# Optimization experiments

Measured on AMD Instinct MI355X. Metric: run time of the kernel, lower is better.

Reference implementation:

```python
import jax, jax.numpy as jnp
import numpy as np

FRAME_LENGTH = 50
MAX_PEOPLE = 3
NEG_INF = -1e10


def _build_smooth_mask():
    tp = FRAME_LENGTH * MAX_PEOPLE
    m = np.zeros((tp, tp), dtype=np.int32)
    for t in range(1, FRAME_LENGTH - 1):
        lo, hi = (t - 1) * MAX_PEOPLE, (t + 1) * MAX_PEOPLE
        m[lo:hi, lo:hi] = 1
    return jnp.asarray(m)


def setup_inputs() -> dict:
    key = jax.random.key(0)
    k1, k2, k3 = jax.random.split(key, 3)
    BS, T, P, H = 32, 50, 3, 4
    TP = T * P
    return {
        "idx": jax.random.randint(k1, (BS, TP), 0, 2),
        "idx_mask": jnp.ones((BS, TP), dtype=jnp.float32),
        "idx_kp": jax.random.randint(jax.random.fold_in(k1, 1), (BS, T, P), 0, 2),
        "points_2d": jax.random.normal(k2, (BS, TP, 44, 2), dtype=jnp.float32),
        "attn": jax.random.normal(k3, (BS, H, TP, TP), dtype=jnp.float32),
    }


def reference(idx, idx_mask, idx_kp, points_2d, attn):
    BS, T, P = idx_kp.shape
    TP = T * P
    kp = points_2d.reshape(BS, TP, 44, 2)
    # pairwise L1 distance summed over keypoints and coords: (BS, TP, TP)
    loss_kp = jnp.sum(jnp.abs(kp[:, None, :, :, :] - kp[:, :, None, :, :]), axis=(3, 4))
    smooth_mask = _build_smooth_mask()  # (TP, TP)
    attn_masked = jnp.where(smooth_mask[None, None] == 0, jnp.asarray(NEG_INF, attn.dtype), attn)
    atten3 = jax.nn.softmax(attn_masked, axis=-1)  # (BS, H, TP, TP)
    smooth_loss = loss_kp[:, None, :, :] * atten3  # (BS, H, TP, TP)
    idx_f = idx.astype(smooth_loss.dtype)
    pair = idx_f[:, None, :, None] * idx_f[:, None, None, :]  # (BS, 1, TP, TP)
    H = attn.shape[1]
    num = jnp.sum(smooth_loss * pair)  # broadcasting over H == masked sum over repeated idx_
    den = 1.0 + H * jnp.sum(pair)      # idx_ was repeated H times before summation
    return num / den
```

## Files before the change

kernel.cpp:

```cpp
#include <hip/hip_runtime.h>
#include <math.h>

#define BS    32
#define T_    50
#define P_    3
#define TP    150
#define HEADS 4
#define NKP   88

__global__ __launch_bounds__(64) void smooth_rows(
    const int*   __restrict__ idx,
    const float* __restrict__ kp,
    const float* __restrict__ attn,
    float*       __restrict__ partials)
{
    int bi = blockIdx.x;
    int b  = bi / TP;
    int i  = bi - b * TP;
    int lane = threadIdx.x;

    if (idx[b * TP + i] == 0) {
        if (lane == 0) partials[bi] = 0.f;
        return;
    }

    const float* kpb = kp + (size_t)b * TP * NKP;

    __shared__ __align__(16) float s_kpi[NKP];
    __shared__ float s_lw[9];

    if (lane < NKP / 2)
        ((float2*)s_kpi)[lane] = ((const float2*)(kpb + i * NKP))[lane];
    __syncthreads();

    if (i < (T_ - 1) * P_) {
        int f   = i / P_;
        int flo = f > 0 ? f - 1 : 0;
        int fhi = f < T_ - 2 ? f + 1 : T_ - 2;
        int jlo = flo * P_;
        int nj  = (fhi - flo + 1) * P_;

        float a0 = s_kpi[lane];
        float a1 = (lane < NKP - 64) ? s_kpi[lane + 64] : 0.f;

        float d[9];
        #pragma unroll
        for (int jj = 0; jj < 9; ++jj) {
            int j = jlo + (jj < nj ? jj : 0);
            const float* kpj = kpb + j * NKP;
            float t = fabsf(kpj[lane] - a0);
            if (lane < NKP - 64) t += fabsf(kpj[lane + 64] - a1);
            d[jj] = t;
        }
        #pragma unroll
        for (int jj = 0; jj < 9; ++jj) {
            #pragma unroll
            for (int off = 32; off; off >>= 1) d[jj] += __shfl_down(d[jj], off);
        }
        if (lane == 0) {
            #pragma unroll
            for (int jj = 0; jj < 9; ++jj) s_lw[jj] = d[jj];
        }
        __syncthreads();

        int h  = lane >> 4;
        int jx = lane & 15;
        bool act = jx < nj;
        int  j  = jlo + (act ? jx : 0);
        float idxj = act ? (float)idx[b * TP + j] : 0.f;
        float a = act ? attn[(((size_t)b * HEADS + h) * TP + i) * TP + j]
                      : -INFINITY;
        float m = a;
        #pragma unroll
        for (int off = 8; off; off >>= 1) m = fmaxf(m, __shfl_xor(m, off));
        float e = act ? expf(a - m) : 0.f;
        float w = act ? e * s_lw[jx] * idxj : 0.f;
        #pragma unroll
        for (int off = 8; off; off >>= 1) { e += __shfl_xor(e, off); w += __shfl_xor(w, off); }
        float ch = w / e;
        float c0 = __shfl(ch, 0);
        float c1 = __shfl(ch, 16);
        float c2 = __shfl(ch, 32);
        float c3 = __shfl(ch, 48);
        if (lane == 0) partials[bi] = c0 + c1 + c2 + c3;
    } else {
        float acc = 0.f;
        for (int j = lane; j < TP; j += 64) {
            if (idx[b * TP + j]) {
                const float4* kpj4 = (const float4*)(kpb + j * NKP);
                const float4* kpi4 = (const float4*)s_kpi;
                float s = 0.f;
                #pragma unroll
                for (int c = 0; c < NKP / 4; ++c) {
                    float4 q = kpj4[c];
                    float4 p = kpi4[c];
                    s += fabsf(q.x - p.x) + fabsf(q.y - p.y)
                       + fabsf(q.z - p.z) + fabsf(q.w - p.w);
                }
                acc += s;
            }
        }
        #pragma unroll
        for (int off = 32; off; off >>= 1) acc += __shfl_down(acc, off);
        if (lane == 0) partials[bi] = acc * ((float)HEADS / (float)TP);
    }
}

__global__ __launch_bounds__(256) void smooth_reduce(
    const int*   __restrict__ idx,
    const float* __restrict__ partials,
    float*       __restrict__ out)
{
    int tid = threadIdx.x;

    float s = 0.f;
    for (int k = tid; k < BS * TP; k += 256) s += partials[k];
    #pragma unroll
    for (int off = 32; off; off >>= 1) s += __shfl_down(s, off);
    __shared__ float s_red[4];
    if ((tid & 63) == 0) s_red[tid >> 6] = s;

    __shared__ int s_sb[BS];
    int b = tid >> 3;
    int l = tid & 7;
    int si = 0;
    for (int k = l; k < TP; k += 8) si += idx[b * TP + k];
    #pragma unroll
    for (int off = 4; off; off >>= 1) si += __shfl_down(si, off, 8);
    if (l == 0) s_sb[b] = si;
    __syncthreads();

    if (tid == 0) {
        float num = s_red[0] + s_red[1] + s_red[2] + s_red[3];
        float tot = 0.f;
        for (int bb = 0; bb < BS; ++bb) {
            float v = (float)s_sb[bb];
            tot += v * v;
        }
        out[0] = num / (1.0f + (float)HEADS * tot);
    }
}

extern "C" void kernel_launch(void* const* d_in, const int* in_sizes, int n_in,
                              void* d_out, int out_size, void* d_ws, size_t ws_size,
                              hipStream_t stream)
{
    const int*   idx  = (const int*)  d_in[0];
    const float* kp   = (const float*)d_in[3];
    const float* attn = (const float*)d_in[4];
    float* out      = (float*)d_out;
    float* partials = (float*)d_ws;

    smooth_rows<<<BS * TP, 64, 0, stream>>>(idx, kp, attn, partials);
    smooth_reduce<<<1, 256, 0, stream>>>(idx, partials, out);
}
```

Measured before the change: 83.73 us.

## Process one frame (three rows) per block, reusing neighbor keypoints in registers

Each block now handles a whole frame of three person rows instead of one row, so the nine neighbor keypoint vectors are loaded once into registers and reused across the three rows. The shared-memory staging and its barrier are replaced by xor-shuffle reductions and register selection. The per-batch idx sum-of-squares now comes from the last-frame block, which simplifies the reduce kernel. The grid shrinks threefold, which lowers parallelism and launch count but raises per-block work and register pressure.

```diff
diff --git a/kernel.cpp b/kernel.cpp
--- a/kernel.cpp
+++ b/kernel.cpp
@@ -7,136 +7,165 @@
 #define TP    150
 #define HEADS 4
 #define NKP   88
+#define NFRM  50
 
-__global__ __launch_bounds__(64) void smooth_rows(
+__global__ __launch_bounds__(64) void smooth_frames(
     const int*   __restrict__ idx,
     const float* __restrict__ kp,
     const float* __restrict__ attn,
     float*       __restrict__ partials)
 {
-    int bi = blockIdx.x;
-    int b  = bi / TP;
-    int i  = bi - b * TP;
+    int bf   = blockIdx.x;
+    int b    = bf / NFRM;
+    int f    = bf - b * NFRM;
     int lane = threadIdx.x;
 
-    if (idx[b * TP + i] == 0) {
-        if (lane == 0) partials[bi] = 0.f;
+    const int*   idxb = idx + b * TP;
+    const float* kpb  = kp + (size_t)b * TP * NKP;
+
+    __shared__ __align__(16) float s_kp[3 * NKP];
+
+    if (f == NFRM - 1) {
+        int si = 0;
+        for (int k = lane; k < TP; k += 64) si += idxb[k];
+        #pragma unroll
+        for (int off = 32; off; off >>= 1) si += __shfl_down(si, off);
+
+        for (int c = lane; c < 3 * NKP / 4; c += 64)
+            ((float4*)s_kp)[c] = ((const float4*)(kpb + (TP - 3) * NKP))[c];
+        __syncthreads();
+
+        int id0 = idxb[TP - 3], id1 = idxb[TP - 2], id2 = idxb[TP - 1];
+
+        float acc0 = 0.f, acc1 = 0.f, acc2 = 0.f;
+        for (int j = lane; j < TP; j += 64) {
+            if (idxb[j]) {
+                const float4* kj = (const float4*)(kpb + j * NKP);
+                const float4* p0 = (const float4*)(s_kp);
+                const float4* p1 = (const float4*)(s_kp + NKP);
+                const float4* p2 = (const float4*)(s_kp + 2 * NKP);
+                float s0 = 0.f, s1 = 0.f, s2 = 0.f;
+                #pragma unroll
+                for (int c = 0; c < NKP / 4; ++c) {
+                    float4 q = kj[c];
+                    float4 a = p0[c];
+                    float4 d = p1[c];
+                    float4 e = p2[c];
+                    s0 += fabsf(q.x - a.x) + fabsf(q.y - a.y) + fabsf(q.z - a.z) + fabsf(q.w - a.w);
+                    s1 += fabsf(q.x - d.x) + fabsf(q.y - d.y) + fabsf(q.z - d.z) + fabsf(q.w - d.w);
+                    s2 += fabsf(q.x - e.x) + fabsf(q.y - e.y) + fabsf(q.z - e.z) + fabsf(q.w - e.w);
+                }
+                acc0 += s0; acc1 += s1; acc2 += s2;
+            }
+        }
+        float acc = (id0 ? acc0 : 0.f) + (id1 ? acc1 : 0.f) + (id2 ? acc2 : 0.f);
+        #pragma unroll
+        for (int off = 32; off; off >>= 1) acc += __shfl_down(acc, off);
+
+        if (lane == 0) {
+            partials[bf] = acc * ((float)HEADS / (float)TP);
+            float fs = (float)si;
+            partials[BS * NFRM + b] = fs * fs;
+        }
         return;
     }
 
-    const float* kpb = kp + (size_t)b * TP * NKP;
+    int i0  = P_ * f;
+    int id0 = idxb[i0], id1 = idxb[i0 + 1], id2 = idxb[i0 + 2];
+    if (!(id0 | id1 | id2)) {
+        if (lane == 0) partials[bf] = 0.f;
+        return;
+    }
 
-    __shared__ __align__(16) float s_kpi[NKP];
-    __shared__ float s_lw[9];
+    int flo = f > 0 ? f - 1 : 0;
+    int fhi = f < T_ - 2 ? f + 1 : T_ - 2;
+    int jlo = flo * P_;
+    int nj  = (fhi - flo + 1) * P_;
 
-    if (lane < NKP / 2)
-        ((float2*)s_kpi)[lane] = ((const float2*)(kpb + i * NKP))[lane];
-    __syncthreads();
+    bool hi = lane < NKP - 64;
+    float kj0[9], kj1[9];
+    #pragma unroll
+    for (int jj = 0; jj < 9; ++jj) {
+        int j = jlo + (jj < nj ? jj : 0);
+        kj0[jj] = kpb[j * NKP + lane];
+        kj1[jj] = hi ? kpb[j * NKP + 64 + lane] : 0.f;
+    }
 
-    if (i < (T_ - 1) * P_) {
-        int f   = i / P_;
-        int flo = f > 0 ? f - 1 : 0;
-        int fhi = f < T_ - 2 ? f + 1 : T_ - 2;
-        int jlo = flo * P_;
-        int nj  = (fhi - flo + 1) * P_;
+    int  h    = lane >> 4;
+    int  jx   = lane & 15;
+    bool act  = jx < nj;
+    float idxj = act ? (float)idxb[jlo + jx] : 0.f;
 
-        float a0 = s_kpi[lane];
-        float a1 = (lane < NKP - 64) ? s_kpi[lane + 64] : 0.f;
+    float acc = 0.f;
+    #pragma unroll
+    for (int ii = 0; ii < 3; ++ii) {
+        int idi = (ii == 0) ? id0 : (ii == 1) ? id1 : id2;
+        if (!idi) continue;
+        int i = i0 + ii;
+
+        float a0 = kpb[i * NKP + lane];
+        float a1 = hi ? kpb[i * NKP + 64 + lane] : 0.f;
 
         float d[9];
         #pragma unroll
-        for (int jj = 0; jj < 9; ++jj) {
-            int j = jlo + (jj < nj ? jj : 0);
-            const float* kpj = kpb + j * NKP;
-            float t = fabsf(kpj[lane] - a0);
-            if (lane < NKP - 64) t += fabsf(kpj[lane + 64] - a1);
-            d[jj] = t;
-        }
+        for (int jj = 0; jj < 9; ++jj)
+            d[jj] = fabsf(kj0[jj] - a0) + fabsf(kj1[jj] - a1);
         #pragma unroll
         for (int jj = 0; jj < 9; ++jj) {
             #pragma unroll
-            for (int off = 32; off; off >>= 1) d[jj] += __shfl_down(d[jj], off);
+            for (int off = 32; off; off >>= 1) d[jj] += __shfl_xor(d[jj], off);
         }
-        if (lane == 0) {
-            #pragma unroll
-            for (int jj = 0; jj < 9; ++jj) s_lw[jj] = d[jj];
-        }
-        __syncthreads();
+        float lw = d[0];
+        lw = (jx == 1) ? d[1] : lw;
+        lw = (jx == 2) ? d[2] : lw;
+        lw = (jx == 3) ? d[3] : lw;
+        lw = (jx == 4) ? d[4] : lw;
+        lw = (jx == 5) ? d[5] : lw;
+        lw = (jx == 6) ? d[6] : lw;
+        lw = (jx == 7) ? d[7] : lw;
+        lw = (jx == 8) ? d[8] : lw;
 
-        int h  = lane >> 4;
-        int jx = lane & 15;
-        bool act = jx < nj;
-        int  j  = jlo + (act ? jx : 0);
-        float idxj = act ? (float)idx[b * TP + j] : 0.f;
-        float a = act ? attn[(((size_t)b * HEADS + h) * TP + i) * TP + j]
+        float a = act ? attn[(((size_t)(b * HEADS + h)) * TP + i) * TP + (jlo + jx)]
                       : -INFINITY;
         float m = a;
         #pragma unroll
         for (int off = 8; off; off >>= 1) m = fmaxf(m, __shfl_xor(m, off));
         float e = act ? expf(a - m) : 0.f;
-        float w = act ? e * s_lw[jx] * idxj : 0.f;
+        float w = e * lw * idxj;
         #pragma unroll
         for (int off = 8; off; off >>= 1) { e += __shfl_xor(e, off); w += __shfl_xor(w, off); }
-        float ch = w / e;
-        float c0 = __shfl(ch, 0);
-        float c1 = __shfl(ch, 16);
-        float c2 = __shfl(ch, 32);
-        float c3 = __shfl(ch, 48);
-        if (lane == 0) partials[bi] = c0 + c1 + c2 + c3;
-    } else {
-        float acc = 0.f;
-        for (int j = lane; j < TP; j += 64) {
-            if (idx[b * TP + j]) {
-                const float4* kpj4 = (const float4*)(kpb + j * NKP);
-                const float4* kpi4 = (const float4*)s_kpi;
-                float s = 0.f;
-                #pragma unroll
-                for (int c = 0; c < NKP / 4; ++c) {
-                    float4 q = kpj4[c];
-                    float4 p = kpi4[c];
-                    s += fabsf(q.x - p.x) + fabsf(q.y - p.y)
-                       + fabsf(q.z - p.z) + fabsf(q.w - p.w);
-                }
-                acc += s;
-            }
-        }
-        #pragma unroll
-        for (int off = 32; off; off >>= 1) acc += __shfl_down(acc, off);
-        if (lane == 0) partials[bi] = acc * ((float)HEADS / (float)TP);
+        acc += w / e;
     }
+
+    float c0 = __shfl(acc, 0);
+    float c1 = __shfl(acc, 16);
+    float c2 = __shfl(acc, 32);
+    float c3 = __shfl(acc, 48);
+    if (lane == 0) partials[bf] = c0 + c1 + c2 + c3;
 }
 
 __global__ __launch_bounds__(256) void smooth_reduce(
-    const int*   __restrict__ idx,
     const float* __restrict__ partials,
     float*       __restrict__ out)
 {
     int tid = threadIdx.x;
 
     float s = 0.f;
-    for (int k = tid; k < BS * TP; k += 256) s += partials[k];
+    for (int k = tid; k < BS * NFRM; k += 256) s += partials[k];
+    float q = (tid < BS) ? partials[BS * NFRM + tid] : 0.f;
+
     #pragma unroll
-    for (int off = 32; off; off >>= 1) s += __shfl_down(s, off);
-    __shared__ float s_red[4];
-    if ((tid & 63) == 0) s_red[tid >> 6] = s;
-
-    __shared__ int s_sb[BS];
-    int b = tid >> 3;
-    int l = tid & 7;
-    int si = 0;
-    for (int k = l; k < TP; k += 8) si += idx[b * TP + k];
-    #pragma unroll
-    for (int off = 4; off; off >>= 1) si += __shfl_down(si, off, 8);
-    if (l == 0) s_sb[b] = si;
+    for (int off = 32; off; off >>= 1) {
+        s += __shfl_down(s, off);
+        q += __shfl_down(q, off);
+    }
+    __shared__ float s_red[4], s_q[4];
+    if ((tid & 63) == 0) { s_red[tid >> 6] = s; s_q[tid >> 6] = q; }
     __syncthreads();
 
     if (tid == 0) {
         float num = s_red[0] + s_red[1] + s_red[2] + s_red[3];
-        float tot = 0.f;
-        for (int bb = 0; bb < BS; ++bb) {
-            float v = (float)s_sb[bb];
-            tot += v * v;
-        }
+        float tot = s_q[0] + s_q[1] + s_q[2] + s_q[3];
         out[0] = num / (1.0f + (float)HEADS * tot);
     }
 }
@@ -151,6 +180,6 @@
     float* out      = (float*)d_out;
     float* partials = (float*)d_ws;
 
-    smooth_rows<<<BS * TP, 64, 0, stream>>>(idx, kp, attn, partials);
-    smooth_reduce<<<1, 256, 0, stream>>>(idx, partials, out);
+    smooth_frames<<<BS * NFRM, 64, 0, stream>>>(idx, kp, attn, partials);
+    smooth_reduce<<<1, 256, 0, stream>>>(partials, out);
 }
```

After: 87.24 us. +4.2%, slower.
